# Optimization experiments

Measured on AMD Instinct MI355X. Metric: run time of the kernel, lower is better.

Reference implementation:

```python
import jax, jax.numpy as jnp
import numpy as np

N_EMBD = 1024
N_HEAD = 16
STRIDE = 128
C = 8
SEQ = 2048
BATCH = 2


def _sparse_causal_mask(nd, ns, stride, c, dtype):
    # Faithful vectorization of _sparse_attention_mask:
    # column j is globally visible if (j % stride) >= stride - c (the last c
    # columns of each stride block), each query also sees its own stride block,
    # and everything is causally masked (j <= q).
    j = jnp.arange(ns)
    q = jnp.arange(ns)[:, None]
    col_sel = (j % stride) >= (stride - c)          # strided summary columns
    same_block = (j[None, :] // stride) == (q // stride)  # local block
    causal = j[None, :] <= q
    mask = ((col_sel[None, :] | same_block) & causal).astype(dtype)
    return mask[ns - nd:]


def setup_inputs() -> dict:
    key = jax.random.key(0)
    k1, k2, k3 = jax.random.split(key, 3)
    inputs = jax.random.normal(k1, (BATCH, SEQ, N_EMBD), dtype=jnp.float32)
    w_attn = jax.random.normal(k2, (N_EMBD, 3 * N_EMBD), dtype=jnp.float32) * 0.02
    b_attn = jnp.zeros((3 * N_EMBD,), dtype=jnp.float32)
    proj_std = 0.02 / np.sqrt(2 * 24)  # n_layer = 24
    w_proj = jax.random.normal(k3, (N_EMBD, N_EMBD), dtype=jnp.float32) * proj_std
    b_proj = jnp.zeros((N_EMBD,), dtype=jnp.float32)
    return {"inputs": inputs, "w_attn": w_attn, "b_attn": b_attn,
            "w_proj": w_proj, "b_proj": b_proj}


def reference(inputs, w_attn, b_attn, w_proj, b_proj):
    B, S, E = inputs.shape
    H = N_HEAD
    D = E // H
    qkv = inputs @ w_attn + b_attn                     # [B,S,3E]
    q, k, v = jnp.split(qkv, 3, axis=-1)
    def split_heads(x):
        return x.reshape(B, S, H, D).transpose(0, 2, 1, 3)  # [B,H,S,D]
    q, k, v = split_heads(q), split_heads(k), split_heads(v)
    present = jnp.stack([k, v], axis=1)                # [B,2,H,S,D]
    scale = jnp.asarray(D, q.dtype) ** 0.5
    w = jnp.einsum('bhqd,bhkd->bhqk', q, k) / scale    # [B,H,S,S]
    mask = _sparse_causal_mask(S, S, STRIDE, C, w.dtype)
    w = w * mask - 1e10 * (1.0 - mask)
    p = jax.nn.softmax(w, axis=-1).astype(v.dtype)
    h = jnp.einsum('bhqk,bhkd->bhqd', p, v)            # [B,H,S,D]
    h = h.transpose(0, 2, 1, 3).reshape(B, S, E)       # merge heads
    h = h @ w_proj + b_proj
    # dropout p=0.0 (eval) -> identity
    return (h, present)
```

## Files before the change

### kernel.cpp

```cpp
#include <hip/hip_runtime.h>
#include <stdint.h>

typedef unsigned short u16;
typedef unsigned int u32;
typedef __attribute__((ext_vector_type(4))) float f32x4;
typedef __attribute__((ext_vector_type(4))) u16 u16x4;
typedef __attribute__((ext_vector_type(8))) __bf16 bf16x8;

__device__ __forceinline__ u16 f2bf(float f) {
  u32 u = __builtin_bit_cast(u32, f);
  u = (u + 0x7FFFu + ((u >> 16) & 1u)) >> 16;
  return (u16)u;
}

__device__ __forceinline__ void gload_lds16(const void* g, void* l) {
  __builtin_amdgcn_global_load_lds(
      (const __attribute__((address_space(1))) void*)(uintptr_t)(g),
      (__attribute__((address_space(3))) void*)(u32)(uintptr_t)(l),
      16, 0, 0);
}

__global__ __launch_bounds__(256) void k_prep(
    const float* __restrict__ x, u16* __restrict__ xbf,
    const float* __restrict__ wa, u16* __restrict__ wat,
    const float* __restrict__ wp, u16* __restrict__ wpt) {
  __shared__ float tile[32][33];
  const int bid = blockIdx.x, t = threadIdx.x;
  if (bid < 4096) {
    int i = bid * 256 + t;
    f32x4 v = ((const f32x4*)x)[i];
    u16x4 o = { f2bf(v.x), f2bf(v.y), f2bf(v.z), f2bf(v.w) };
    ((u16x4*)xbf)[i] = o;
    return;
  }
  const float* in;
  u16* out;
  int n0, k0, N;
  if (bid < 4096 + 3072) {
    int idx = bid - 4096;
    in = wa; out = wat; N = 3072;
    n0 = (idx % 96) * 32; k0 = (idx / 96) * 32;
  } else {
    int idx = bid - 7168;
    in = wp; out = wpt; N = 1024;
    n0 = (idx & 31) * 32; k0 = (idx >> 5) * 32;
  }
  int c = t & 31, r0 = t >> 5;
#pragma unroll
  for (int i = 0; i < 4; ++i)
    tile[r0 + i * 8][c] = in[(size_t)(k0 + r0 + i * 8) * N + n0 + c];
  __syncthreads();
  int on = t >> 3, ok = (t & 7) * 4;
  u16x4 o = { f2bf(tile[ok + 0][on]), f2bf(tile[ok + 1][on]),
              f2bf(tile[ok + 2][on]), f2bf(tile[ok + 3][on]) };
  *(u16x4*)&out[(size_t)(n0 + on) * 1024 + k0 + ok] = o;
}

__global__ __launch_bounds__(256) void k_kv(const float* __restrict__ present,
                                            u16* __restrict__ kbf,
                                            u16* __restrict__ vtw) {
  __shared__ float tile[32][33];
  const int bid = blockIdx.x, t = threadIdx.x;
  if (bid >= 4096) {
    int i = bid - 4096;
    size_t idx = (size_t)i * 256 + t;
    size_t b = idx >> 19, off = idx & ((1u << 19) - 1);
    f32x4 v = ((const f32x4*)present)[b * (1u << 20) + off];
    u16x4 o = { f2bf(v.x), f2bf(v.y), f2bf(v.z), f2bf(v.w) };
    ((u16x4*)kbf)[idx] = o;
    return;
  }
  int bh = bid >> 7, rem = bid & 127;
  int s0 = (rem >> 1) * 32, d0 = (rem & 1) * 32;
  int b = bh >> 4, h = bh & 15;
  const float* vsrc = present + (((size_t)(b * 2 + 1) * 16 + h) * 2048) * 64;
  u16* vdst = vtw + ((size_t)bh * 64) * 2048;
  int c = t & 31, r0 = t >> 5;
#pragma unroll
  for (int i = 0; i < 4; ++i)
    tile[r0 + i * 8][c] = vsrc[(size_t)(s0 + r0 + i * 8) * 64 + d0 + c];
  __syncthreads();
  int on = t >> 3, ok = (t & 7) * 4;
  u16x4 o = { f2bf(tile[ok + 0][on]), f2bf(tile[ok + 1][on]),
              f2bf(tile[ok + 2][on]), f2bf(tile[ok + 3][on]) };
  *(u16x4*)&vdst[(size_t)(d0 + on) * 2048 + s0 + ok] = o;
}

template <int EPI, int BN>
__global__ __launch_bounds__(256) void k_gemm(
    const u16* __restrict__ A, const u16* __restrict__ Bt,
    const float* __restrict__ bias, u16* __restrict__ outq,
    float* __restrict__ outp, int M, int N, int K) {
  __shared__ u16 a_lds[128 * 64];
  __shared__ u16 b_lds[BN * 64];
  const int t = threadIdx.x;
  const int lane = t & 63, w = t >> 6;
  const int m0 = blockIdx.y * 128, n0 = blockIdx.x * BN;
  const int srow = t >> 3;
  const int scb = (t & 7) * 16;
  const int ssw = scb ^ ((srow & 7) << 4);
  const size_t pitch = (size_t)K * 2;
  const char* aS = (const char*)A + (size_t)(m0 + srow) * pitch + ssw;
  const char* bS = (const char*)Bt + (size_t)(n0 + srow) * pitch + ssw;
  char* al = (char*)a_lds + t * 16;
  char* bl = (char*)b_lds + t * 16;
  const int wm = (w >> 1) * 64, wn = (w & 1) * (BN / 2);
  const int cc = lane & 15, g = lane >> 4;
  constexpr int NF = BN / 32;

  f32x4 acc[4][NF] = {};

  for (int kt = 0; kt < K; kt += 64) {
    __syncthreads();
#pragma unroll
    for (int i = 0; i < 4; ++i)
      gload_lds16(aS + (size_t)kt * 2 + (size_t)i * 32 * pitch, al + i * 4096);
#pragma unroll
    for (int i = 0; i < BN / 32; ++i)
      gload_lds16(bS + (size_t)kt * 2 + (size_t)i * 32 * pitch, bl + i * 4096);
    __syncthreads();
#pragma unroll
    for (int kk = 0; kk < 2; ++kk) {
      bf16x8 af[4], bf_[NF];
#pragma unroll
      for (int mf = 0; mf < 4; ++mf) {
        int row = wm + mf * 16 + cc;
        af[mf] = *(const bf16x8*)((const char*)a_lds + row * 128 +
                                  ((kk * 64 + g * 16) ^ ((row & 7) << 4)));
      }
#pragma unroll
      for (int nf = 0; nf < NF; ++nf) {
        int row = wn + nf * 16 + cc;
        bf_[nf] = *(const bf16x8*)((const char*)b_lds + row * 128 +
                                   ((kk * 64 + g * 16) ^ ((row & 7) << 4)));
      }
#pragma unroll
      for (int mf = 0; mf < 4; ++mf)
#pragma unroll
        for (int nf = 0; nf < NF; ++nf)
          acc[mf][nf] = __builtin_amdgcn_mfma_f32_16x16x32_bf16(
              af[mf], bf_[nf], acc[mf][nf], 0, 0, 0);
    }
  }

  float bv[NF];
#pragma unroll
  for (int nf = 0; nf < NF; ++nf) bv[nf] = bias[n0 + wn + nf * 16 + cc];

#pragma unroll
  for (int mf = 0; mf < 4; ++mf)
#pragma unroll
    for (int nf = 0; nf < NF; ++nf) {
      int n = n0 + wn + nf * 16 + cc;
      int mb = m0 + wm + mf * 16 + g * 4;
      float v[4];
#pragma unroll
      for (int j = 0; j < 4; ++j) v[j] = acc[mf][nf][j] + bv[nf];
      if (EPI == 1) {
#pragma unroll
        for (int j = 0; j < 4; ++j) outp[(size_t)(mb + j) * N + n] = v[j];
      } else if (n < 1024) {
#pragma unroll
        for (int j = 0; j < 4; ++j) outq[(size_t)(mb + j) * 1024 + n] = f2bf(v[j]);
      } else {
        int n2 = n - 1024;
        int kv = n2 >> 10; n2 &= 1023;
        int hh = n2 >> 6, d = n2 & 63;
        int bb = mb >> 11, ss = mb & 2047;
        float* pr = outp + ((((size_t)bb * 2 + kv) * 16 + hh) * 2048 + ss) * 64 + d;
#pragma unroll
        for (int j = 0; j < 4; ++j) pr[(size_t)j * 64] = v[j];
      }
    }
}

__global__ __launch_bounds__(256) void k_attn(
    const u16* __restrict__ qws, const u16* __restrict__ kbf,
    const u16* __restrict__ vtw, u16* __restrict__ hws) {
  const int qb = blockIdx.x, h = blockIdx.y, b = blockIdx.z;
  const int t = threadIdx.x, lane = t & 63, w = t >> 6;
  const int cc = lane & 15, g = lane >> 4;

  __shared__ u16 k_lds[256 * 64];
  __shared__ u16 p_lds[4][32 * 72];
  __shared__ float rsum[4][32];

  const char* kh = (const char*)kbf + (size_t)(b * 16 + h) * (2048 * 128);
  const char* vh = (const char*)vtw + (size_t)(b * 16 + h) * (64 * 4096);

  {
    int rr = t >> 3, seg = (t & 7) * 16;
#pragma unroll
    for (int i = 0; i < 8; ++i) {
      int r = i * 32 + rr;
      int i2 = r - 128;
      int gr = (r < 128) ? (qb * 128 + r) : ((i2 >> 3) * 128 + 120 + (i2 & 7));
      gload_lds16(kh + (size_t)gr * 128 + (seg ^ ((r & 7) << 4)),
                  (char*)k_lds + i * 4096 + t * 16);
    }
  }

  bf16x8 qf_[2][2];
  {
    const char* qsrc = (const char*)qws +
        (size_t)(b * 2048 + qb * 128 + w * 32 + cc) * 2048 + h * 128 + g * 16;
#pragma unroll
    for (int qf = 0; qf < 2; ++qf)
#pragma unroll
      for (int kk = 0; kk < 2; ++kk)
        qf_[qf][kk] = *(const bf16x8*)(qsrc + (size_t)qf * 16 * 2048 + kk * 64);
  }
  __syncthreads();

  const int nsum = 8 * qb;
  f32x4 o_[2][4] = {};
  float lsum[2] = { 0.f, 0.f };

#pragma unroll 2
  for (int ch = 0; ch < 4; ++ch) {
    f32x4 s[4][2] = {};
#pragma unroll
    for (int kf2 = 0; kf2 < 4; ++kf2) {
      int row = ch * 64 + kf2 * 16 + cc;
      const char* kr = (const char*)k_lds + row * 128;
#pragma unroll
      for (int kk = 0; kk < 2; ++kk) {
        bf16x8 kfr = *(const bf16x8*)(kr + ((kk * 64 + g * 16) ^ ((cc & 7) << 4)));
#pragma unroll
        for (int qf = 0; qf < 2; ++qf)
          s[kf2][qf] = __builtin_amdgcn_mfma_f32_16x16x32_bf16(
              kfr, qf_[qf][kk], s[kf2][qf], 0, 0, 0);
      }
    }
#pragma unroll
    for (int qf = 0; qf < 2; ++qf) {
      int q_local = w * 32 + qf * 16 + cc;
#pragma unroll
      for (int kf2 = 0; kf2 < 4; ++kf2) {
#pragma unroll
        for (int j = 0; j < 4; ++j) {
          int key = ch * 64 + kf2 * 16 + g * 4 + j;
          bool vis = (key < 128) ? (key <= q_local) : (key - 128 < nsum);
          float p = vis ? exp2f(s[kf2][qf][j] * 0.180336884f) : 0.f;
          s[kf2][qf][j] = p;
          lsum[qf] += p;
        }
        u16x4 pw = { f2bf(s[kf2][qf][0]), f2bf(s[kf2][qf][1]),
                     f2bf(s[kf2][qf][2]), f2bf(s[kf2][qf][3]) };
        *(u16x4*)&p_lds[w][(qf * 16 + cc) * 72 + kf2 * 16 + g * 4] = pw;
      }
    }
#pragma unroll
    for (int kk = 0; kk < 2; ++kk) {
      bf16x8 pa[2], vb[4];
#pragma unroll
      for (int mf = 0; mf < 2; ++mf)
        pa[mf] = *(const bf16x8*)((const char*)p_lds[w] +
                                  (mf * 16 + cc) * 144 + kk * 64 + g * 16);
      int cb = (ch < 2) ? (qb * 256 + ch * 128 + kk * 64 + g * 16)
                        : (((ch - 2) * 8 + kk * 4 + g) * 256 + 240);
#pragma unroll
      for (int nf = 0; nf < 4; ++nf)
        vb[nf] = *(const bf16x8*)(vh + (size_t)(nf * 16 + cc) * 4096 + cb);
#pragma unroll
      for (int mf = 0; mf < 2; ++mf)
#pragma unroll
        for (int nf = 0; nf < 4; ++nf)
          o_[mf][nf] = __builtin_amdgcn_mfma_f32_16x16x32_bf16(pa[mf], vb[nf],
                                                               o_[mf][nf], 0, 0, 0);
    }
  }

#pragma unroll
  for (int qf = 0; qf < 2; ++qf) {
    float sum = lsum[qf];
    sum += __shfl_xor(sum, 16);
    sum += __shfl_xor(sum, 32);
    if (g == 0) rsum[w][qf * 16 + cc] = sum;
  }
#pragma unroll
  for (int mf = 0; mf < 2; ++mf)
#pragma unroll
    for (int j = 0; j < 4; ++j) {
      float inv = 1.0f / rsum[w][mf * 16 + g * 4 + j];
      size_t row = (size_t)(b * 2048 + qb * 128 + w * 32 + mf * 16 + g * 4 + j);
#pragma unroll
      for (int nf = 0; nf < 4; ++nf)
        hws[row * 1024 + h * 64 + nf * 16 + cc] = f2bf(o_[mf][nf][j] * inv);
    }
}

extern "C" void kernel_launch(void* const* d_in, const int* in_sizes, int n_in,
                              void* d_out, int out_size, void* d_ws, size_t ws_size,
                              hipStream_t stream) {
  const float* x      = (const float*)d_in[0];
  const float* w_attn = (const float*)d_in[1];
  const float* b_attn = (const float*)d_in[2];
  const float* w_proj = (const float*)d_in[3];
  const float* b_proj = (const float*)d_in[4];
  float* h_out   = (float*)d_out;
  float* present = (float*)d_out + 4194304;

  char* ws = (char*)d_ws;
  u16* xbf = (u16*)(ws);
  u16* qws = (u16*)(ws + (8u << 20));
  u16* wat = (u16*)(ws + (16u << 20));
  u16* wpt = (u16*)(ws + (22u << 20));
  u16* kbf = (u16*)(ws + (24u << 20));
  u16* vtw = (u16*)(ws + (32u << 20));
  u16* hws = xbf;

  k_prep<<<8192, 256, 0, stream>>>(x, xbf, w_attn, wat, w_proj, wpt);
  k_gemm<0, 128><<<dim3(24, 32), 256, 0, stream>>>(xbf, wat, b_attn, qws,
                                                   present, 4096, 3072, 1024);
  k_kv<<<8192, 256, 0, stream>>>(present, kbf, vtw);
  k_attn<<<dim3(16, 16, 2), 256, 0, stream>>>(qws, kbf, vtw, hws);
  k_gemm<1, 64><<<dim3(16, 32), 256, 0, stream>>>(hws, wpt, b_proj, nullptr,
                                                  h_out, 4096, 1024, 1024);
}
```

Baseline: 91.99 us.

## Use 256x256 double-buffered tile GEMM for QKV projection

Replaces the 128x128 QKV GEMM with a dedicated 512-thread kernel that computes 256x256 output tiles. It double-buffers LDS with direct global-to-LDS loads and swizzles block order for L2 locality. Larger tiles raise operand reuse and overlap loads with MFMA work, but launch only 192 blocks, which leaves some CUs idle. It also uses a large LDS footprint that limits the kernel to one block per CU.

New measurement: 92.40 us. No clear change (+0.4%).

```diff
diff --git a/kernel.cpp b/kernel.cpp
--- a/kernel.cpp
+++ b/kernel.cpp
@@ -84,6 +84,111 @@
   u16x4 o = { f2bf(tile[ok + 0][on]), f2bf(tile[ok + 1][on]),
               f2bf(tile[ok + 2][on]), f2bf(tile[ok + 3][on]) };
   *(u16x4*)&vdst[(size_t)(d0 + on) * 2048 + s0 + ok] = o;
+}
+
+__global__ __launch_bounds__(512, 1) void k_gemm256(
+    const u16* __restrict__ A, const u16* __restrict__ Bt,
+    const float* __restrict__ bias, u16* __restrict__ outq,
+    float* __restrict__ outp) {
+  __shared__ u16 a_lds[2][256 * 64];
+  __shared__ u16 b_lds[2][256 * 64];
+  const int t = threadIdx.x;
+  const int lane = t & 63, w = t >> 6;
+  const int cc = lane & 15, g = lane >> 4;
+  const int wr = w >> 2, wc = w & 3;
+
+  int flat = blockIdx.y * 12 + blockIdx.x;
+  flat = (flat & 7) * 24 + (flat >> 3);
+  const int m0 = (flat / 12) * 256, n0 = (flat % 12) * 256;
+
+  const int srow = t >> 3;
+  const int scolb = (t & 7) * 16;
+  const size_t pitch = 2048;
+
+  auto stage = [&](int bi, int kt) {
+#pragma unroll
+    for (int hh = 0; hh < 2; ++hh)
+#pragma unroll
+      for (int i = 0; i < 2; ++i) {
+        int row = hh * 128 + i * 64 + srow;
+        int sw = scolb ^ ((row & 7) << 4);
+        gload_lds16((const char*)A + (size_t)(m0 + row) * pitch + kt * 128 + sw,
+                    (char*)a_lds[bi] + row * 128 + scolb);
+        gload_lds16((const char*)Bt + (size_t)(n0 + row) * pitch + kt * 128 + sw,
+                    (char*)b_lds[bi] + row * 128 + scolb);
+      }
+  };
+
+  f32x4 acc[8][4] = {};
+
+  stage(0, 0);
+  stage(1, 1);
+  __syncthreads();
+
+  for (int kt = 0; kt < 16; ++kt) {
+    const int bi = kt & 1;
+    if (kt >= 1 && kt < 15) stage(1 - bi, kt + 1);
+
+    bf16x8 bfr[4][2];
+#pragma unroll
+    for (int nf = 0; nf < 4; ++nf) {
+      int row = wc * 64 + nf * 16 + cc;
+#pragma unroll
+      for (int kk = 0; kk < 2; ++kk)
+        bfr[nf][kk] = *(const bf16x8*)((const char*)b_lds[bi] + row * 128 +
+                                       ((kk * 64 + g * 16) ^ ((row & 7) << 4)));
+    }
+#pragma unroll
+    for (int q = 0; q < 4; ++q) {
+      bf16x8 af[2][2];
+#pragma unroll
+      for (int mf = 0; mf < 2; ++mf) {
+        int row = wr * 128 + q * 32 + mf * 16 + cc;
+#pragma unroll
+        for (int kk = 0; kk < 2; ++kk)
+          af[mf][kk] = *(const bf16x8*)((const char*)a_lds[bi] + row * 128 +
+                                        ((kk * 64 + g * 16) ^ ((row & 7) << 4)));
+      }
+      __builtin_amdgcn_s_setprio(1);
+#pragma unroll
+      for (int mf = 0; mf < 2; ++mf)
+#pragma unroll
+        for (int nf = 0; nf < 4; ++nf)
+#pragma unroll
+          for (int kk = 0; kk < 2; ++kk)
+            acc[q * 2 + mf][nf] = __builtin_amdgcn_mfma_f32_16x16x32_bf16(
+                af[mf][kk], bfr[nf][kk], acc[q * 2 + mf][nf], 0, 0, 0);
+      __builtin_amdgcn_s_setprio(0);
+    }
+    if (kt < 15) __syncthreads();
+  }
+
+  float bv[4];
+#pragma unroll
+  for (int nf = 0; nf < 4; ++nf) bv[nf] = bias[n0 + wc * 64 + nf * 16 + cc];
+
+#pragma unroll
+  for (int q8 = 0; q8 < 8; ++q8)
+#pragma unroll
+    for (int nf = 0; nf < 4; ++nf) {
+      int n = n0 + wc * 64 + nf * 16 + cc;
+      int mb = m0 + wr * 128 + q8 * 16 + g * 4;
+      float v[4];
+#pragma unroll
+      for (int j = 0; j < 4; ++j) v[j] = acc[q8][nf][j] + bv[nf];
+      if (n < 1024) {
+#pragma unroll
+        for (int j = 0; j < 4; ++j) outq[(size_t)(mb + j) * 1024 + n] = f2bf(v[j]);
+      } else {
+        int n2 = n - 1024;
+        int kv = n2 >> 10; n2 &= 1023;
+        int hh = n2 >> 6, d = n2 & 63;
+        int bb = mb >> 11, ss = mb & 2047;
+        float* pr = outp + ((((size_t)bb * 2 + kv) * 16 + hh) * 2048 + ss) * 64 + d;
+#pragma unroll
+        for (int j = 0; j < 4; ++j) pr[(size_t)j * 64] = v[j];
+      }
+    }
 }
 
 template <int EPI, int BN>
@@ -311,8 +416,7 @@
   u16* hws = xbf;
 
   k_prep<<<8192, 256, 0, stream>>>(x, xbf, w_attn, wat, w_proj, wpt);
-  k_gemm<0, 128><<<dim3(24, 32), 256, 0, stream>>>(xbf, wat, b_attn, qws,
-                                                   present, 4096, 3072, 1024);
+  k_gemm256<<<dim3(12, 16), 512, 0, stream>>>(xbf, wat, b_attn, qws, present);
   k_kv<<<8192, 256, 0, stream>>>(present, kbf, vtw);
   k_attn<<<dim3(16, 16, 2), 256, 0, stream>>>(qws, kbf, vtw, hws);
   k_gemm<1, 64><<<dim3(16, 32), 256, 0, stream>>>(hws, wpt, b_proj, nullptr,
```
